# Performance work log

Hardware: AMD Instinct MI355X
Metric: run time of the kernel (lower is better)

## Reference

```python
import jax, jax.numpy as jnp
import numpy as np
from jax.ops import segment_sum

N_NODE, N_EDGE, D_IN, D_HID, N_CLS = 50000, 800000, 64, 64, 40


def setup_inputs() -> dict:
    key = jax.random.key(0)
    k1, k2, k3, k4 = jax.random.split(key, 4)
    x = jax.random.normal(k1, (N_NODE, D_IN), dtype=jnp.float32)
    edge_index = jax.random.randint(k2, (2, N_EDGE), 0, N_NODE, dtype=jnp.int64)
    W1 = jax.random.normal(k3, (D_IN, D_HID), dtype=jnp.float32) * (1.0 / np.sqrt(D_IN))
    b1 = jnp.zeros((D_HID,), dtype=jnp.float32)
    W2 = jax.random.normal(k4, (D_HID, N_CLS), dtype=jnp.float32) * (1.0 / np.sqrt(D_HID))
    b2 = jnp.zeros((N_CLS,), dtype=jnp.float32)
    return {"x": x, "edge_index": edge_index, "W1": W1, "b1": b1, "W2": W2, "b2": b2}


def _att_weights(fea, row, col, n):
    # edge-parallel cosine similarity (sklearn cosine_similarity restricted to edges)
    nrm = jnp.sqrt(jnp.sum(fea * fea, axis=1, keepdims=True))
    fn = fea / jnp.maximum(nrm, 1e-12)
    sim = jnp.sum(fn[row] * fn[col], axis=1)                 # [E]
    sim = jnp.where(sim < 0.1, 0.0, sim)                      # threshold
    # L1 row-normalization (sim >= 0 after threshold)
    rs = segment_sum(sim, row, num_segments=n)                # [N]
    sim_n = jnp.where(sim > 0, sim / jnp.maximum(rs[row], 1e-12), 0.0)
    # degree-based self-loop weight lam = 1/(deg+1)
    deg = segment_sum((sim > 0).astype(fea.dtype), row, num_segments=n)
    lam = 1.0 / (deg + 1.0)
    # exp applied only to stored (nonzero) entries; zeroed edges stay 0
    w_edge = jnp.where(sim > 0, jnp.exp(sim_n), 0.0)          # [E]
    w_self = jnp.exp(lam)                                     # [N] self-loop weights
    return w_edge, w_self


def _gcn(h, W, b, row, col, w_edge, w_self, n):
    # symmetric-norm GCN over weighted edges + explicit self loops
    deg = segment_sum(w_edge, row, num_segments=n) + w_self
    dinv = 1.0 / jnp.sqrt(jnp.maximum(deg, 1e-12))
    h = h @ W                                                 # [N, F]
    coef = w_edge * dinv[row] * dinv[col]                     # [E]
    out = segment_sum(coef[:, None] * h[col], row, num_segments=n)
    out = out + (w_self * dinv * dinv)[:, None] * h + b
    return out


def reference(x, edge_index, W1, b1, W2, b2):
    n = x.shape[0]
    row, col = edge_index[0], edge_index[1]
    # layer 1: attention coefs from raw features
    w1e, w1s = _att_weights(x, row, col, n)
    h = jax.nn.relu(_gcn(x, W1, b1, row, col, w1e, w1s, n))
    # layer 2: attention coefs recomputed on hidden features (dropout = eval mode)
    w2e, w2s = _att_weights(h, row, col, n)
    out = _gcn(h, W2, b2, row, col, w2e, w2s, n)
    return jax.nn.log_softmax(out, axis=1)
```

## Files before the change

### kernel.cpp

```cpp
#include <hip/hip_runtime.h>
#include <math.h>


#define ATT_CAP 96
#define EPB     2048
#define RPB     128
#define NBUCK_MAX 512
#define CAPB    4096

typedef _Float16 half4 __attribute__((ext_vector_type(4)));

__global__ void k_bscat_norm_gemm(const int* __restrict__ row, const int* __restrict__ col,
                                  int* __restrict__ gcur, int* __restrict__ ebuf,
                                  int E, int nbuck, int nblkA, int nblkB,
                                  const float* __restrict__ x, float* __restrict__ fn,
                                  const float* __restrict__ W1, float* __restrict__ hd1,
                                  int N)
{
    __shared__ int lh[NBUCK_MAX];
    __shared__ int lbase[NBUCK_MAX];
    __shared__ float sW[64 * 64];
    __shared__ float sX[4 * 64];
    int b = blockIdx.x;
    int tid = threadIdx.x;
    if (b >= nblkA + nblkB) {
        int gb = b - nblkA - nblkB;
        const float4* W4 = (const float4*)W1;
        float4* s4 = (float4*)sW;
#pragma unroll
        for (int i = 0; i < 4; ++i) s4[tid + 256 * i] = W4[tid + 256 * i];
        int base = gb * 4;
        {
            int rr = base + (tid >> 6);
            sX[tid] = (rr < N) ? x[(unsigned)rr * 64u + (unsigned)(tid & 63)] : 0.0f;
        }
        __syncthreads();
        int rl = tid >> 6, j = tid & 63;
        int r = base + rl;
        if (r < N) {
            float acc = 0.0f;
#pragma unroll
            for (int k = 0; k < 64; ++k) acc = fmaf(sX[rl * 64 + k], sW[k * 64 + j], acc);
            hd1[(unsigned)r * 64u + (unsigned)j] = acc;
        }
        return;
    }
    if (b >= nblkA) {
        int gid  = (b - nblkA) * blockDim.x + tid;
        int wid  = gid >> 6;
        int lane = tid & 63;
        if (wid >= N) return;
        float v = x[(unsigned)wid * 64u + (unsigned)lane];
        float s = v * v;
#pragma unroll
        for (int off = 32; off > 0; off >>= 1) s += __shfl_xor(s, off);
        float inv = rsqrtf(fmaxf(s, 1e-24f));
        fn[(unsigned)wid * 64u + (unsigned)lane] = v * inv;
        return;
    }
    int ebeg = b * EPB;
    int rr[8], cc[8];
    for (int i = tid; i < nbuck; i += blockDim.x) lh[i] = 0;
    __syncthreads();
#pragma unroll
    for (int k = 0; k < 8; ++k) {
        int e = ebeg + k * 256 + tid;
        bool v = (e < E);
        int r = v ? row[e] : -1;
        int c = v ? col[e] : 0;
        rr[k] = r; cc[k] = c;
        if (v) atomicAdd(&lh[r >> 7], 1);
    }
    __syncthreads();
    for (int i = tid; i < nbuck; i += blockDim.x) {
        int cnt = lh[i];
        if (cnt) lbase[i] = i * CAPB + atomicAdd(gcur + i, cnt);
        lh[i] = 0;
    }
    __syncthreads();
#pragma unroll
    for (int k = 0; k < 8; ++k) {
        int r = rr[k];
        if (r >= 0) {
            int j = r >> 7;
            int pos = lbase[j] + atomicAdd(&lh[j], 1);
            ebuf[pos] = ((r & (RPB - 1)) << 16) | cc[k];
        }
    }
}

__global__ void k_csr(const int* __restrict__ ebuf, const int* __restrict__ gcur,
                      int* __restrict__ rptr, int* __restrict__ col_s,
                      int N, int E, int nbuck)
{
    __shared__ int pk[CAPB];
    __shared__ int lcol[CAPB];
    __shared__ int lcnt[RPB], lexc[RPB], lcur[RPB];
    __shared__ int spart[4];
    int j = blockIdx.x;
    int tid = threadIdx.x;
    int lane = tid & 63, wave = tid >> 6;

    int part = 0;
    for (int i = tid; i < j; i += blockDim.x) part += gcur[i];
#pragma unroll
    for (int off = 32; off > 0; off >>= 1) part += __shfl_xor(part, off);
    if (lane == 0) spart[wave] = part;
    if (tid < RPB) lcnt[tid] = 0;
    __syncthreads();
    int beg = spart[0] + spart[1] + spart[2] + spart[3];
    int m = gcur[j]; if (m > CAPB) m = CAPB;

    const int* seg = ebuf + (size_t)j * CAPB;
    for (int i = tid; i < m; i += blockDim.x) pk[i] = seg[i];
    __syncthreads();
    for (int i = tid; i < m; i += blockDim.x) atomicAdd(&lcnt[pk[i] >> 16], 1);
    __syncthreads();
    if (tid < 64) {
        int a = lcnt[2 * tid], b2 = lcnt[2 * tid + 1];
        int s = a + b2;
        int incl = s;
#pragma unroll
        for (int off = 1; off < 64; off <<= 1) {
            int v = __shfl_up(incl, off);
            if (tid >= off) incl += v;
        }
        int base = incl - s;
        lexc[2 * tid] = base;     lexc[2 * tid + 1] = base + a;
        lcur[2 * tid] = base;     lcur[2 * tid + 1] = base + a;
    }
    __syncthreads();
    for (int i = tid; i < m; i += blockDim.x) {
        int v = pk[i];
        int p = atomicAdd(&lcur[v >> 16], 1);
        lcol[p] = v & 0xFFFF;
    }
    __syncthreads();
    for (int i = tid; i < m; i += blockDim.x) col_s[beg + i] = lcol[i];
    if (tid < RPB) {
        int r = j * RPB + tid;
        if (r < N) rptr[r] = beg + lexc[tid];
    }
    if (j == 0 && tid == 0) rptr[N] = E;
}

__global__ void k_att(const float* __restrict__ fn,
                      const int* __restrict__ rptr, const int* __restrict__ col_s,
                      int2* __restrict__ cw, int* __restrict__ lend,
                      float* __restrict__ dinv, float* __restrict__ selfc,
                      const float* __restrict__ g2, _Float16* __restrict__ hd2,
                      float* __restrict__ hsc, int n)
{
    __shared__ float ssim[4][ATT_CAP];
    __shared__ int   scol[4][ATT_CAP];
    int wib  = threadIdx.x >> 6;
    int wid  = blockIdx.x * 4 + wib;
    int lane = threadIdx.x & 63;
    if (wid >= n) return;
    int sub = lane & 3;
    int grp = lane >> 2;
    int beg = rptr[wid], end = rptr[wid + 1];
    int deg_all = end - beg;

    const float4* frp = (const float4*)fn;
    unsigned rbase = (unsigned)wid * 16u;
    float4 a0 = frp[rbase + sub],     a1 = frp[rbase + sub + 4],
           a2 = frp[rbase + sub + 8], a3 = frp[rbase + sub + 12];

    float rs_part = 0.0f;
    int ngrp = (deg_all + 15) >> 4;
    for (int g = 0; g < ngrp; ++g) {
        int li = g * 16 + grp;
        float s = 0.0f; int c = 0;
        bool valid = (li < deg_all);
        if (valid) {
            c = col_s[beg + li];
            unsigned cb = (unsigned)c * 16u;
            float4 b0 = frp[cb + sub],     b1 = frp[cb + sub + 4],
                   b2 = frp[cb + sub + 8], b3 = frp[cb + sub + 12];
            float p = a0.x * b0.x + a0.y * b0.y + a0.z * b0.z + a0.w * b0.w
                    + a1.x * b1.x + a1.y * b1.y + a1.z * b1.z + a1.w * b1.w
                    + a2.x * b2.x + a2.y * b2.y + a2.z * b2.z + a2.w * b2.w
                    + a3.x * b3.x + a3.y * b3.y + a3.z * b3.z + a3.w * b3.w;
            p += __shfl_xor(p, 1);
            p += __shfl_xor(p, 2);
            s = (p < 0.1f) ? 0.0f : p;
        }
        if (sub == 0 && valid) {
            if (li < ATT_CAP) { ssim[wib][li] = s; scol[wib][li] = c; }
            if (s > 0.0f) rs_part += s;
        }
    }
#pragma unroll
    for (int off = 32; off > 0; off >>= 1) rs_part += __shfl_xor(rs_part, off);
    float denom = fmaxf(rs_part, 1e-12f);

    int   nlive = 0;
    float sw_lane = 0.0f;
    for (int base = 0; base < deg_all; base += 64) {
        int li = base + lane;
        bool valid = (li < deg_all);
        float s = 0.0f; int c = 0;
        if (valid) {
            if (li < ATT_CAP) { s = ssim[wib][li]; c = scol[wib][li]; }
            else {
                c = col_s[beg + li];
                const float* fr = fn + (size_t)wid * 64;
                const float* fc = fn + (size_t)c * 64;
                float p = 0.0f;
                for (int k = 0; k < 64; ++k) p += fr[k] * fc[k];
                s = (p < 0.1f) ? 0.0f : p;
            }
        }
        float w = (valid && s > 0.0f) ? __expf(s / denom) : 0.0f;
        unsigned long long M = __ballot(w > 0.0f);
        int rank = __popcll(M & ((1ull << lane) - 1ull));
        if (w > 0.0f) {
            int2 pw; pw.x = c; pw.y = __float_as_int(w);
            cw[beg + nlive + rank] = pw;
            sw_lane += w;
        }
        nlive += __popcll(M);
    }
#pragma unroll
    for (int off = 32; off > 0; off >>= 1) sw_lane += __shfl_xor(sw_lane, off);

    float wself = __expf(1.0f / ((float)nlive + 1.0f));
    float D  = sw_lane + wself;
    float di = rsqrtf(fmaxf(D, 1e-12f));
    if (lane == 0) {
        lend[wid]  = beg + nlive;
        dinv[wid]  = di;
        selfc[wid] = wself * di;
    }
    if (hsc)
        hsc[(unsigned)wid * 64u + (unsigned)lane] *= di;
    if (g2 && lane < 40)
        hd2[(unsigned)wid * 40u + (unsigned)lane] =
            (_Float16)(g2[(unsigned)wid * 40u + (unsigned)lane] * di);
}

template <int F, typename Vec4>
__device__ inline float agg_core_t(const Vec4* __restrict__ hdv,
                                   const int2* __restrict__ cw,
                                   int beg, int lend_, int lane)
{
    int q  = lane & 15;
    int eg = lane >> 4;
    bool qact = (F == 64) ? true : (q < (F >> 2));
    constexpr unsigned FQ = F >> 2;
    float acc0 = 0.f, acc1 = 0.f, acc2 = 0.f, acc3 = 0.f;
    for (int base = beg; base < lend_; base += 64) {
        int idx = base + lane;
        int cv = 0; float wv = 0.0f;
        if (idx < lend_) { int2 pw = cw[(unsigned)idx]; cv = pw.x; wv = __int_as_float(pw.y); }
        int cnt = lend_ - base; if (cnt > 64) cnt = 64;
        int nit = (cnt + 3) >> 2;

        Vec4  hv[4] = {};
        float wj[4] = {};
#pragma unroll
        for (int p = 0; p < 4; ++p) {
            int c = __shfl(cv, 4 * p + eg);
            wj[p] = __shfl(wv, 4 * p + eg);
            if (qact && p < nit) hv[p] = hdv[(unsigned)c * FQ + (unsigned)q];
        }
#pragma unroll
        for (int it = 0; it < 16; ++it) {
            if (it < nit) {
                float w = wj[it & 3];
                Vec4  h = hv[it & 3];
                acc0 += w * (float)h.x;
                acc1 += w * (float)h.y;
                acc2 += w * (float)h.z;
                acc3 += w * (float)h.w;
                if (it + 4 < nit) {
                    int jn = 4 * (it + 4);
                    int c = __shfl(cv, jn + eg);
                    wj[it & 3] = __shfl(wv, jn + eg);
                    if (qact) hv[it & 3] = hdv[(unsigned)c * FQ + (unsigned)q];
                }
            }
        }
    }
    acc0 += __shfl_xor(acc0, 16); acc0 += __shfl_xor(acc0, 32);
    acc1 += __shfl_xor(acc1, 16); acc1 += __shfl_xor(acc1, 32);
    acc2 += __shfl_xor(acc2, 16); acc2 += __shfl_xor(acc2, 32);
    acc3 += __shfl_xor(acc3, 16); acc3 += __shfl_xor(acc3, 32);
    int srcq = lane >> 2;
    float a0 = __shfl(acc0, srcq);
    float a1 = __shfl(acc1, srcq);
    float a2 = __shfl(acc2, srcq);
    float a3 = __shfl(acc3, srcq);
    int k = lane & 3;
    return (k == 0) ? a0 : (k == 1) ? a1 : (k == 2) ? a2 : a3;
}

__global__ void k_agg64(const float* __restrict__ hd, const int2* __restrict__ cw,
                        const float* __restrict__ dinv, const float* __restrict__ selfc,
                        const float* __restrict__ b, const int* __restrict__ row_ptr,
                        const int* __restrict__ lend, const float* __restrict__ W2,
                        float* __restrict__ g2, float* __restrict__ fnh, int n)
{
    __shared__ float sW2[64 * 40];
    __shared__ float sv[4][64];
    int tid = threadIdx.x;
    {
        const float4* W4 = (const float4*)W2;
        float4* s4 = (float4*)sW2;
        for (int i = tid; i < 64 * 40 / 4; i += 256) s4[i] = W4[i];
    }
    __syncthreads();

    int lane = tid & 63;
    int wib  = tid >> 6;
    float bl = b[lane];
    for (int t = 0; t < 2; ++t) {
        int wid = blockIdx.x * 8 + wib * 2 + t;
        if (wid >= n) break;
        int beg = row_ptr[wid], le = lend[wid];
        float hs = hd[(unsigned)wid * 64u + (unsigned)lane];
        float dv = dinv[wid];
        float sc = selfc[wid];
        float accf = agg_core_t<64>((const float4*)hd, cw, beg, le, lane);
        float v = dv * accf + sc * hs + bl;
        v = fmaxf(v, 0.0f);
        float s = v * v;
#pragma unroll
        for (int off = 32; off > 0; off >>= 1) s += __shfl_xor(s, off);
        float inv = rsqrtf(fmaxf(s, 1e-24f));
        fnh[(unsigned)wid * 64u + (unsigned)lane] = v * inv;

        sv[wib][lane] = v;
        if (lane < 40) {
            float acc = 0.0f;
#pragma unroll
            for (int k = 0; k < 64; ++k) acc = fmaf(sv[wib][k], sW2[k * 40 + lane], acc);
            g2[(unsigned)wid * 40u + (unsigned)lane] = acc;
        }
    }
}

__global__ void k_agg40_lsm(const _Float16* __restrict__ hd2, const int2* __restrict__ cw,
                            const float* __restrict__ dinv, const float* __restrict__ selfc,
                            const float* __restrict__ b, const int* __restrict__ row_ptr,
                            const int* __restrict__ lend,
                            float* __restrict__ out, int n)
{
    constexpr int F = 40;
    int gid  = blockIdx.x * blockDim.x + threadIdx.x;
    int wid  = gid >> 6;
    int lane = threadIdx.x & 63;
    if (wid >= n) return;
    int beg = row_ptr[wid], le = lend[wid];
    bool active = (lane < F);
    float hs = active ? (float)hd2[(unsigned)wid * 40u + (unsigned)lane] : 0.0f;
    float dv = dinv[wid];
    float sc = selfc[wid];
    float bl = active ? b[lane] : 0.0f;
    float accf = agg_core_t<F>((const half4*)hd2, cw, beg, le, lane);
    float v = 0.0f;
    if (active) v = dv * accf + sc * hs + bl;
    float m = active ? v : -__builtin_inff();
#pragma unroll
    for (int off = 32; off > 0; off >>= 1) m = fmaxf(m, __shfl_xor(m, off));
    float ex = active ? __expf(v - m) : 0.0f;
    float s = ex;
#pragma unroll
    for (int off = 32; off > 0; off >>= 1) s += __shfl_xor(s, off);
    if (active) out[(size_t)wid * F + lane] = v - m - __logf(s);
}

extern "C" void kernel_launch(void* const* d_in, const int* in_sizes, int n_in,
                              void* d_out, int out_size, void* d_ws, size_t ws_size,
                              hipStream_t stream)
{
    const float* x  = (const float*)d_in[0];
    const int*   ei = (const int*)d_in[1];
    const float* W1 = (const float*)d_in[2];
    const float* b1 = (const float*)d_in[3];
    const float* W2 = (const float*)d_in[4];
    const float* b2 = (const float*)d_in[5];
    float* out = (float*)d_out;

    const int N = in_sizes[0] / 64;
    const int E = in_sizes[1] / 2;
    const int* row = ei;
    const int* col = ei + E;

    const int nblkA = (E + EPB - 1) / EPB;
    const int nbuck = (N + RPB - 1) / RPB;

    char* p = (char*)d_ws;
    auto alloc = [&](size_t bytes) -> char* {
        char* r = p; p += (bytes + 255) & ~(size_t)255; return r;
    };
    float*     fn     = (float*)alloc((size_t)N * 64 * 4);
    float*     dinv   = (float*)alloc((size_t)N * 4);
    float*     selfc  = (float*)alloc((size_t)N * 4);
    float*     hd1    = (float*)alloc((size_t)N * 64 * 4);
    float*     g2     = (float*)alloc((size_t)N * 40 * 4);
    _Float16*  hd2    = (_Float16*)alloc((size_t)N * 40 * 2);
    float*     fnh    = (float*)alloc((size_t)N * 64 * 4);
    int*       rptr   = (int*)alloc((size_t)(N + 1) * 4);
    int*       lendv  = (int*)alloc((size_t)N * 4);
    int*       col_s  = (int*)alloc((size_t)E * 4);
    int2*      cw     = (int2*)alloc((size_t)E * 8);
    int*       ebuf   = (int*)alloc((size_t)nbuck * CAPB * 4);
    int*       gcur   = (int*)alloc((size_t)nbuck * 4);

    const int TB = 256;
    int blk_nodeWave = (N * 64 + TB - 1) / TB;
    int blk_gemm     = (N + 3) / 4;
    int blk_node4    = (N + 3) / 4;
    int blk_node8    = (N + 7) / 8;

    hipMemsetAsync(gcur, 0, (size_t)nbuck * 4, stream);

    k_bscat_norm_gemm<<<nblkA + blk_nodeWave + blk_gemm, TB, 0, stream>>>(
        row, col, gcur, ebuf, E, nbuck, nblkA, blk_nodeWave, x, fn, W1, hd1, N);
    k_csr<<<nbuck, TB, 0, stream>>>(ebuf, gcur, rptr, col_s, N, E, nbuck);

    k_att<<<blk_node4, TB, 0, stream>>>(fn, rptr, col_s, cw, lendv, dinv, selfc,
                                        (const float*)nullptr, (_Float16*)nullptr,
                                        hd1, N);
    k_agg64<<<blk_node8, TB, 0, stream>>>(hd1, cw, dinv, selfc, b1,
                                          rptr, lendv, W2, g2, fnh, N);

    k_att<<<blk_node4, TB, 0, stream>>>(fnh, rptr, col_s, cw, lendv, dinv, selfc,
                                        g2, hd2, (float*)nullptr, N);
    k_agg40_lsm<<<blk_nodeWave, TB, 0, stream>>>(hd2, cw, dinv, selfc, b2,
                                                 rptr, lendv, out, N);
}
```

Baseline: 251.9 us.

## Replace bucketed two-pass CSR build with degree count, scan, and atomic scatter

Builds the CSR adjacency differently. Per-node degrees are counted with global atomics, fused into the existing normalize/GEMM kernel. A single 1024-thread block then scans them into row pointers, and a separate kernel scatters column indices through per-node atomic cursors. This drops the bucket staging buffer, the fixed per-bucket capacity cap, and the shared-memory local sort. The cost is an extra launch, a serial single-block scan over 50k nodes, and many contended global atomics. Column order within each row is now nondeterministic.

```diff
diff --git a/kernel.cpp b/kernel.cpp
--- a/kernel.cpp
+++ b/kernel.cpp
@@ -3,50 +3,31 @@
 
 
 #define ATT_CAP 96
-#define EPB     2048
-#define RPB     128
-#define NBUCK_MAX 512
-#define CAPB    4096
 
 typedef _Float16 half4 __attribute__((ext_vector_type(4)));
 
-__global__ void k_bscat_norm_gemm(const int* __restrict__ row, const int* __restrict__ col,
-                                  int* __restrict__ gcur, int* __restrict__ ebuf,
-                                  int E, int nbuck, int nblkA, int nblkB,
-                                  const float* __restrict__ x, float* __restrict__ fn,
-                                  const float* __restrict__ W1, float* __restrict__ hd1,
-                                  int N)
-{
-    __shared__ int lh[NBUCK_MAX];
-    __shared__ int lbase[NBUCK_MAX];
+__global__ void k_deg_norm_gemm(const int* __restrict__ row,
+                                int* __restrict__ deg,
+                                int E, int nblkD, int nblkB,
+                                const float* __restrict__ x, float* __restrict__ fn,
+                                const float* __restrict__ W1, float* __restrict__ hd1,
+                                int N)
+{
     __shared__ float sW[64 * 64];
     __shared__ float sX[4 * 64];
     int b = blockIdx.x;
     int tid = threadIdx.x;
-    if (b >= nblkA + nblkB) {
-        int gb = b - nblkA - nblkB;
-        const float4* W4 = (const float4*)W1;
-        float4* s4 = (float4*)sW;
-#pragma unroll
-        for (int i = 0; i < 4; ++i) s4[tid + 256 * i] = W4[tid + 256 * i];
-        int base = gb * 4;
-        {
-            int rr = base + (tid >> 6);
-            sX[tid] = (rr < N) ? x[(unsigned)rr * 64u + (unsigned)(tid & 63)] : 0.0f;
-        }
-        __syncthreads();
-        int rl = tid >> 6, j = tid & 63;
-        int r = base + rl;
-        if (r < N) {
-            float acc = 0.0f;
-#pragma unroll
-            for (int k = 0; k < 64; ++k) acc = fmaf(sX[rl * 64 + k], sW[k * 64 + j], acc);
-            hd1[(unsigned)r * 64u + (unsigned)j] = acc;
+    if (b < nblkD) {
+        int e0 = b * 512 + tid;
+#pragma unroll
+        for (int k = 0; k < 2; ++k) {
+            int e = e0 + k * 256;
+            if (e < E) atomicAdd(&deg[row[e]], 1);
         }
         return;
     }
-    if (b >= nblkA) {
-        int gid  = (b - nblkA) * blockDim.x + tid;
+    if (b < nblkD + nblkB) {
+        int gid  = (b - nblkD) * blockDim.x + tid;
         int wid  = gid >> 6;
         int lane = tid & 63;
         if (wid >= N) return;
@@ -58,90 +39,71 @@
         fn[(unsigned)wid * 64u + (unsigned)lane] = v * inv;
         return;
     }
-    int ebeg = b * EPB;
-    int rr[8], cc[8];
-    for (int i = tid; i < nbuck; i += blockDim.x) lh[i] = 0;
+    int gb = b - nblkD - nblkB;
+    const float4* W4 = (const float4*)W1;
+    float4* s4 = (float4*)sW;
+#pragma unroll
+    for (int i = 0; i < 4; ++i) s4[tid + 256 * i] = W4[tid + 256 * i];
+    int base = gb * 4;
+    {
+        int rr = base + (tid >> 6);
+        sX[tid] = (rr < N) ? x[(unsigned)rr * 64u + (unsigned)(tid & 63)] : 0.0f;
+    }
     __syncthreads();
-#pragma unroll
-    for (int k = 0; k < 8; ++k) {
-        int e = ebeg + k * 256 + tid;
-        bool v = (e < E);
-        int r = v ? row[e] : -1;
-        int c = v ? col[e] : 0;
-        rr[k] = r; cc[k] = c;
-        if (v) atomicAdd(&lh[r >> 7], 1);
-    }
+    int rl = tid >> 6, j = tid & 63;
+    int r = base + rl;
+    if (r < N) {
+        float acc = 0.0f;
+#pragma unroll
+        for (int k = 0; k < 64; ++k) acc = fmaf(sX[rl * 64 + k], sW[k * 64 + j], acc);
+        hd1[(unsigned)r * 64u + (unsigned)j] = acc;
+    }
+}
+
+__global__ void k_scan(const int* __restrict__ deg, int* __restrict__ rptr,
+                       int* __restrict__ cur, int N, int E)
+{
+    __shared__ int wsum[16];
+    int tid = threadIdx.x;
+    int lane = tid & 63, w = tid >> 6;
+    const int C = (N + 1023) / 1024;
+    int s0 = tid * C;
+    int s1 = s0 + C; if (s1 > N) s1 = N;
+    int lsum = 0;
+    for (int i = s0; i < s1; ++i) lsum += deg[i];
+    int incl = lsum;
+#pragma unroll
+    for (int off = 1; off < 64; off <<= 1) {
+        int v = __shfl_up(incl, off);
+        if (lane >= off) incl += v;
+    }
+    if (lane == 63) wsum[w] = incl;
     __syncthreads();
-    for (int i = tid; i < nbuck; i += blockDim.x) {
-        int cnt = lh[i];
-        if (cnt) lbase[i] = i * CAPB + atomicAdd(gcur + i, cnt);
-        lh[i] = 0;
-    }
-    __syncthreads();
-#pragma unroll
-    for (int k = 0; k < 8; ++k) {
-        int r = rr[k];
-        if (r >= 0) {
-            int j = r >> 7;
-            int pos = lbase[j] + atomicAdd(&lh[j], 1);
-            ebuf[pos] = ((r & (RPB - 1)) << 16) | cc[k];
-        }
-    }
-}
-
-__global__ void k_csr(const int* __restrict__ ebuf, const int* __restrict__ gcur,
-                      int* __restrict__ rptr, int* __restrict__ col_s,
-                      int N, int E, int nbuck)
-{
-    __shared__ int pk[CAPB];
-    __shared__ int lcol[CAPB];
-    __shared__ int lcnt[RPB], lexc[RPB], lcur[RPB];
-    __shared__ int spart[4];
-    int j = blockIdx.x;
-    int tid = threadIdx.x;
-    int lane = tid & 63, wave = tid >> 6;
-
-    int part = 0;
-    for (int i = tid; i < j; i += blockDim.x) part += gcur[i];
-#pragma unroll
-    for (int off = 32; off > 0; off >>= 1) part += __shfl_xor(part, off);
-    if (lane == 0) spart[wave] = part;
-    if (tid < RPB) lcnt[tid] = 0;
-    __syncthreads();
-    int beg = spart[0] + spart[1] + spart[2] + spart[3];
-    int m = gcur[j]; if (m > CAPB) m = CAPB;
-
-    const int* seg = ebuf + (size_t)j * CAPB;
-    for (int i = tid; i < m; i += blockDim.x) pk[i] = seg[i];
-    __syncthreads();
-    for (int i = tid; i < m; i += blockDim.x) atomicAdd(&lcnt[pk[i] >> 16], 1);
-    __syncthreads();
-    if (tid < 64) {
-        int a = lcnt[2 * tid], b2 = lcnt[2 * tid + 1];
-        int s = a + b2;
-        int incl = s;
-#pragma unroll
-        for (int off = 1; off < 64; off <<= 1) {
-            int v = __shfl_up(incl, off);
-            if (tid >= off) incl += v;
-        }
-        int base = incl - s;
-        lexc[2 * tid] = base;     lexc[2 * tid + 1] = base + a;
-        lcur[2 * tid] = base;     lcur[2 * tid + 1] = base + a;
-    }
-    __syncthreads();
-    for (int i = tid; i < m; i += blockDim.x) {
-        int v = pk[i];
-        int p = atomicAdd(&lcur[v >> 16], 1);
-        lcol[p] = v & 0xFFFF;
-    }
-    __syncthreads();
-    for (int i = tid; i < m; i += blockDim.x) col_s[beg + i] = lcol[i];
-    if (tid < RPB) {
-        int r = j * RPB + tid;
-        if (r < N) rptr[r] = beg + lexc[tid];
-    }
-    if (j == 0 && tid == 0) rptr[N] = E;
+    int wbase = 0;
+    for (int j = 0; j < w; ++j) wbase += wsum[j];
+    int run = wbase + incl - lsum;
+    for (int i = s0; i < s1; ++i) {
+        int d = deg[i];
+        rptr[i] = run;
+        cur[i]  = run;
+        run += d;
+    }
+    if (tid == 0) rptr[N] = E;
+}
+
+__global__ void k_scatter(const int* __restrict__ row, const int* __restrict__ col,
+                          int* __restrict__ cur, int* __restrict__ col_s, int E)
+{
+    int e0 = blockIdx.x * 512 + threadIdx.x;
+#pragma unroll
+    for (int k = 0; k < 2; ++k) {
+        int e = e0 + k * 256;
+        if (e < E) {
+            int r = row[e], c = col[e];
+            int pos = atomicAdd(&cur[r], 1);
+            col_s[pos] = c;
+        }
+    }
 }
 
 __global__ void k_att(const float* __restrict__ fn,
@@ -388,9 +350,6 @@
     const int* row = ei;
     const int* col = ei + E;
 
-    const int nblkA = (E + EPB - 1) / EPB;
-    const int nbuck = (N + RPB - 1) / RPB;
-
     char* p = (char*)d_ws;
     auto alloc = [&](size_t bytes) -> char* {
         char* r = p; p += (bytes + 255) & ~(size_t)255; return r;
@@ -406,20 +365,22 @@
     int*       lendv  = (int*)alloc((size_t)N * 4);
     int*       col_s  = (int*)alloc((size_t)E * 4);
     int2*      cw     = (int2*)alloc((size_t)E * 8);
-    int*       ebuf   = (int*)alloc((size_t)nbuck * CAPB * 4);
-    int*       gcur   = (int*)alloc((size_t)nbuck * 4);
+    int*       deg    = (int*)alloc((size_t)N * 4);
+    int*       cur    = (int*)alloc((size_t)N * 4);
 
     const int TB = 256;
     int blk_nodeWave = (N * 64 + TB - 1) / TB;
     int blk_gemm     = (N + 3) / 4;
     int blk_node4    = (N + 3) / 4;
     int blk_node8    = (N + 7) / 8;
-
-    hipMemsetAsync(gcur, 0, (size_t)nbuck * 4, stream);
-
-    k_bscat_norm_gemm<<<nblkA + blk_nodeWave + blk_gemm, TB, 0, stream>>>(
-        row, col, gcur, ebuf, E, nbuck, nblkA, blk_nodeWave, x, fn, W1, hd1, N);
-    k_csr<<<nbuck, TB, 0, stream>>>(ebuf, gcur, rptr, col_s, N, E, nbuck);
+    int nblkD        = (E + 511) / 512;
+
+    hipMemsetAsync(deg, 0, (size_t)N * 4, stream);
+
+    k_deg_norm_gemm<<<nblkD + blk_nodeWave + blk_gemm, TB, 0, stream>>>(
+        row, deg, E, nblkD, blk_nodeWave, x, fn, W1, hd1, N);
+    k_scan<<<1, 1024, 0, stream>>>(deg, rptr, cur, N, E);
+    k_scatter<<<nblkD, TB, 0, stream>>>(row, col, cur, col_s, E);
 
     k_att<<<blk_node4, TB, 0, stream>>>(fn, rptr, col_s, cw, lendv, dinv, selfc,
                                         (const float*)nullptr, (_Float16*)nullptr,
```

New measurement: 417.7 us. +65.8%, slower.
